# Optimization experiments

Measured on AMD Instinct MI355X. Metric: run time of the kernel, lower is better.

Reference implementation:

```python
import jax, jax.numpy as jnp
import numpy as np

B, S, E, H, K, V = 2, 2048, 2048, 16, 128, 128
EPS = 1e-5


def _rotate(x, cos, sin):
    half = K // 2
    swapped = jnp.concatenate((x[..., half:], x[..., :half]), axis=-1)
    return cos * x + sin * swapped


def setup_inputs() -> dict:
    key = jax.random.key(0)
    k1, k2, k3 = jax.random.split(key, 3)
    embeddings = jax.random.normal(k1, (B, S, E), jnp.float32)
    pos = jnp.arange(S, dtype=jnp.float32)[:, None]
    inv_freq = 1.0 / (10000.0 ** (jnp.arange(0, K, 2, dtype=jnp.float32) / K))
    ang = pos * inv_freq[None, :]
    ang = jnp.concatenate((ang, ang), axis=-1)
    cosb = jnp.cos(ang)[None, None, :, :]
    sinb = jnp.sin(ang)[None, None, :, :]
    cos_buffer = jnp.stack((cosb, cosb))
    sin_buffer = jnp.stack((sinb, sinb))
    causal_buffer = jnp.tril(jnp.ones((S, S), dtype=bool))[None, None]
    w_norm = jnp.ones((E,), jnp.float32)
    w_qkv = jax.random.normal(k2, (E, 2 * K * H + V * H), jnp.float32) * 0.02
    w_out = jax.random.normal(k3, (H * V, E), jnp.float32) * 0.02
    return dict(embeddings=embeddings, cos_buffer=cos_buffer, sin_buffer=sin_buffer,
                causal_buffer=causal_buffer, w_norm=w_norm, w_qkv=w_qkv, w_out=w_out)


def reference(embeddings, cos_buffer, sin_buffer, causal_buffer, w_norm, w_qkv, w_out):
    ms = jnp.mean(embeddings * embeddings, axis=-1, keepdims=True)
    normed = embeddings * jax.lax.rsqrt(ms + EPS) * w_norm
    qkv = normed @ w_qkv
    ks = K * H
    q = qkv[..., :ks].reshape(B, S, H, K).transpose(0, 2, 1, 3)
    k = qkv[..., ks:2 * ks].reshape(B, S, H, K).transpose(0, 2, 1, 3)
    v = qkv[..., 2 * ks:].reshape(B, S, H, V).transpose(0, 2, 1, 3)
    present_k, present_v = k, v
    q = _rotate(q, cos_buffer[0], sin_buffer[0])
    k = _rotate(k, cos_buffer[1], sin_buffer[1])
    scores = jnp.einsum('bhqk,bhsk->bhqs', q, k) / np.float32(np.sqrt(K))
    scores = jnp.where(causal_buffer, scores, -jnp.inf)
    attn = jax.nn.softmax(scores, axis=-1)
    out = jnp.einsum('bhqs,bhsv->bhqv', attn, v)
    out = out.transpose(0, 2, 1, 3).reshape(B, S, H * V) @ w_out
    return embeddings + out, present_k, present_v
```

## Files before the change

kernel.cpp:

```cpp
#include <hip/hip_runtime.h>

typedef unsigned short u16;
typedef unsigned int   u32;
typedef short bf16x8 __attribute__((ext_vector_type(8)));
typedef float f32x4  __attribute__((ext_vector_type(4)));
typedef float f4     __attribute__((ext_vector_type(4)));
typedef u16   u16x4  __attribute__((ext_vector_type(4)));
typedef u16   u16x8  __attribute__((ext_vector_type(8)));

__device__ __forceinline__ u16 f2bf(float x) {
  u32 u = __float_as_uint(x);
  u += 0x7fff + ((u >> 16) & 1);
  return (u16)(u >> 16);
}
__device__ __forceinline__ float bf2f(u16 h) {
  return __uint_as_float(((u32)h) << 16);
}
__device__ __forceinline__ void gload16(const void* g, void* l) {
  __builtin_amdgcn_global_load_lds((const __attribute__((address_space(1))) u32*)g,
                                   (__attribute__((address_space(3))) u32*)l, 16, 0, 0);
}
__device__ __forceinline__ f32x4 mfma16(bf16x8 a, bf16x8 b, f32x4 c) {
  return __builtin_amdgcn_mfma_f32_16x16x32_bf16(a, b, c, 0, 0, 0);
}

__global__ __launch_bounds__(256) void k_rmsnorm(const float* __restrict__ x,
                                                 const float* __restrict__ w,
                                                 u16* __restrict__ out) {
  const int row = blockIdx.x, tid = threadIdx.x;
  const float* xr = x + (size_t)row * 2048;
  f4 a = *(const f4*)&xr[tid * 8];
  f4 b = *(const f4*)&xr[tid * 8 + 4];
  float ss = a[0]*a[0]+a[1]*a[1]+a[2]*a[2]+a[3]*a[3]+b[0]*b[0]+b[1]*b[1]+b[2]*b[2]+b[3]*b[3];
#pragma unroll
  for (int off = 32; off > 0; off >>= 1) ss += __shfl_xor(ss, off);
  __shared__ float red[4];
  if ((tid & 63) == 0) red[tid >> 6] = ss;
  __syncthreads();
  ss = red[0] + red[1] + red[2] + red[3];
  const float sc = rsqrtf(ss * (1.0f / 2048.0f) + 1e-5f);
  f4 wa = *(const f4*)&w[tid * 8];
  f4 wb = *(const f4*)&w[tid * 8 + 4];
  u16x8 o;
#pragma unroll
  for (int i = 0; i < 4; ++i) o[i] = f2bf(a[i] * sc * wa[i]);
#pragma unroll
  for (int i = 0; i < 4; ++i) o[4 + i] = f2bf(b[i] * sc * wb[i]);
  *(u16x8*)&out[(size_t)row * 2048 + tid * 8] = o;
}

__global__ __launch_bounds__(256) void k_transpose_cvt(const float* __restrict__ src,
                                                       u16* __restrict__ dst,
                                                       int R, int C) {
  __shared__ float t[32][33];
  const int tid = threadIdx.x;
  const size_t zoff = (size_t)blockIdx.z * (size_t)R * (size_t)C;
  src += zoff; dst += zoff;
  const int r0 = blockIdx.y * 32, c0 = blockIdx.x * 32;
  const int rr = tid >> 3, cc = (tid & 7) * 4;
  f4 v = *(const f4*)&src[(size_t)(r0 + rr) * C + c0 + cc];
  t[rr][cc] = v[0]; t[rr][cc + 1] = v[1]; t[rr][cc + 2] = v[2]; t[rr][cc + 3] = v[3];
  __syncthreads();
  const int oc = tid >> 3, orr = (tid & 7) * 4;
  u16x4 o;
#pragma unroll
  for (int k = 0; k < 4; ++k) o[k] = f2bf(t[orr + k][oc]);
  *(u16x4*)&dst[(size_t)(c0 + oc) * R + r0 + orr] = o;
}

template <int EPI>
__global__ __launch_bounds__(256) void k_gemm128(
    const u16* __restrict__ A, const u16* __restrict__ Bt,
    u16* __restrict__ q_pre, float* __restrict__ outK, float* __restrict__ outV,
    const float* __restrict__ emb, float* __restrict__ out0,
    u16* __restrict__ vtf) {
  constexpr int KD = 2048;
  __shared__ __align__(16) u16 lA[128 * 64];
  __shared__ __align__(16) u16 lB[128 * 64];
  const int tid = threadIdx.x;
  const int lane = tid & 63;
  const int w = tid >> 6;
  const int wr = w >> 1, wc = w & 1;
  const int g = lane >> 4, c15 = lane & 15;
  const int m0 = blockIdx.y * 128, n0 = blockIdx.x * 128;
  f32x4 acc[4][4] = {};
  for (int kt = 0; kt < KD / 64; ++kt) {
    __syncthreads();
#pragma unroll
    for (int p = 0; p < 4; ++p) {
      int c = p * 256 + tid;
      int row = c >> 3, ch = c & 7;
      int gch = ch ^ (row & 7);
      gload16(&A[(size_t)(m0 + row) * KD + kt * 64 + gch * 8], &lA[c * 8]);
      gload16(&Bt[(size_t)(n0 + row) * KD + kt * 64 + gch * 8], &lB[c * 8]);
    }
    __syncthreads();
#pragma unroll
    for (int ks = 0; ks < 2; ++ks) {
      bf16x8 af[4], bfr[4];
#pragma unroll
      for (int i = 0; i < 4; ++i) {
        int row = wr * 64 + i * 16 + c15;
        int chn = (ks * 4 + g) ^ (row & 7);
        af[i] = *(const bf16x8*)&lA[row * 64 + chn * 8];
      }
#pragma unroll
      for (int j = 0; j < 4; ++j) {
        int row = wc * 64 + j * 16 + c15;
        int chn = (ks * 4 + g) ^ (row & 7);
        bfr[j] = *(const bf16x8*)&lB[row * 64 + chn * 8];
      }
#pragma unroll
      for (int i = 0; i < 4; ++i)
#pragma unroll
        for (int j = 0; j < 4; ++j)
          acc[i][j] = mfma16(af[i], bfr[j], acc[i][j]);
    }
  }
  const int rb = m0 + wr * 64 + g * 4;
  const int cb = wc * 64 + c15;
  if (EPI == 0) {
    const int sec = n0 >> 11;
    const int h = (n0 & 2047) >> 7;
#pragma unroll
    for (int i = 0; i < 4; ++i)
#pragma unroll
      for (int j = 0; j < 4; ++j) {
        const int d = cb + j * 16;
        const int mb = rb + i * 16;
        const int b_ = mb >> 11, s0 = mb & 2047;
#pragma unroll
        for (int r = 0; r < 4; ++r) {
          size_t o = ((size_t)(b_ * 16 + h) * 2048 + (s0 + r)) * 128 + d;
          float val = acc[i][j][r];
          if (sec == 0)      q_pre[o] = f2bf(val);
          else if (sec == 1) outK[o] = val;
          else               outV[o] = val;
        }
        if (sec == 2 && vtf != nullptr) {
          u16x4 vt;
#pragma unroll
          for (int r = 0; r < 4; ++r) vt[r] = f2bf(acc[i][j][r]);
          *(u16x4*)&vtf[((size_t)(b_ * 16 + h) * 128 + d) * 2048 + s0] = vt;
        }
      }
  } else {
#pragma unroll
    for (int i = 0; i < 4; ++i)
#pragma unroll
      for (int j = 0; j < 4; ++j)
#pragma unroll
        for (int r = 0; r < 4; ++r) {
          int mm = rb + i * 16 + r;
          int nn = n0 + cb + j * 16;
          size_t o = (size_t)mm * 2048 + nn;
          out0[o] = acc[i][j][r] + emb[o];
        }
  }
}

__global__ __launch_bounds__(256) void k_rope(const u16* __restrict__ qp,
                                              const float* __restrict__ kp,
                                              const float* __restrict__ cosb,
                                              const float* __restrict__ sinb,
                                              u16* __restrict__ qr, u16* __restrict__ kr) {
  const int gid = blockIdx.x * 256 + threadIdx.x;
  const int row = gid >> 4;
  const int d0 = (gid & 15) * 4;
  const int s = row & 2047;
  const float SC = 0.08838834764831845f;
  const float* c1 = cosb + (size_t)s * 128;
  const float* s1 = sinb + (size_t)s * 128;
  const float* c2 = c1 + 262144;
  const float* s2 = s1 + 262144;
  const size_t base = (size_t)row * 128;
  f4 cl = *(const f4*)&c1[d0], ch = *(const f4*)&c1[d0 + 64];
  f4 sl = *(const f4*)&s1[d0], sh = *(const f4*)&s1[d0 + 64];
  {
    u16x4 xl = *(const u16x4*)&qp[base + d0];
    u16x4 xh = *(const u16x4*)&qp[base + d0 + 64];
    u16x4 ol, oh;
#pragma unroll
    for (int i = 0; i < 4; ++i) {
      float lo = bf2f(xl[i]), hi = bf2f(xh[i]);
      ol[i] = f2bf((cl[i] * lo + sl[i] * hi) * SC);
      oh[i] = f2bf((ch[i] * hi + sh[i] * lo) * SC);
    }
    *(u16x4*)&qr[base + d0] = ol;
    *(u16x4*)&qr[base + d0 + 64] = oh;
  }
  {
    f4 c2l = *(const f4*)&c2[d0], c2h = *(const f4*)&c2[d0 + 64];
    f4 s2l = *(const f4*)&s2[d0], s2h = *(const f4*)&s2[d0 + 64];
    f4 xl = *(const f4*)&kp[base + d0];
    f4 xh = *(const f4*)&kp[base + d0 + 64];
    u16x4 ol, oh;
#pragma unroll
    for (int i = 0; i < 4; ++i) {
      ol[i] = f2bf(c2l[i] * xl[i] + s2l[i] * xh[i]);
      oh[i] = f2bf(c2h[i] * xh[i] + s2h[i] * xl[i]);
    }
    *(u16x4*)&kr[base + d0] = ol;
    *(u16x4*)&kr[base + d0 + 64] = oh;
  }
}

__device__ __forceinline__ void stage_kv(const u16* kb, const u16* vb, int kv0,
                                         u16* dK, u16* dV, int tid) {
#pragma unroll
  for (int p = 0; p < 4; ++p) {
    int c = p * 256 + tid;
    { int row = c >> 4, ch = c & 15, gch = ch ^ (row & 7);
      gload16(&kb[(size_t)(kv0 + row) * 128 + gch * 8], &dK[c * 8]); }
    { int row = c >> 3, ch = c & 7, gch = ch ^ (row & 7);
      gload16(&vb[(size_t)row * 2048 + kv0 + gch * 8], &dV[c * 8]); }
  }
}

__global__ __launch_bounds__(256) void k_attn(const u16* __restrict__ q_rot,
                                              const u16* __restrict__ k_rot,
                                              const u16* __restrict__ v_t,
                                              u16* __restrict__ attn_o) {
  const int bh = blockIdx.y;
  const int b = bh >> 4, h = bh & 15;
  const int tid = threadIdx.x, w = tid >> 6, lane = tid & 63;
  const int g = lane >> 4, c15 = lane & 15;
  __shared__ __align__(16) u16 lK[2][64 * 128];
  __shared__ __align__(16) u16 lV[2][128 * 64];
  __shared__ __align__(16) u16 lP[4][16 * 64];

  const u16* qb = q_rot + (size_t)bh * 2048 * 128;
  const u16* kb = k_rot + (size_t)bh * 2048 * 128;
  const u16* vb = v_t + (size_t)bh * 128 * 2048;
  const float L2E = 1.442695040888963f;
  const float SHIFT = 11.541560327111707f;

  for (int halfp = 0; halfp < 2; ++halfp) {
    const int qt = halfp ? (int)blockIdx.x : 31 - (int)blockIdx.x;
    const int q0 = qt * 64;
    const int nt = qt + 1;

    bf16x8 qf[4];
    const int qrow = q0 + w * 16 + c15;
#pragma unroll
    for (int f = 0; f < 4; ++f)
      qf[f] = *(const bf16x8*)&qb[(size_t)qrow * 128 + f * 32 + g * 8];

    f32x4 O[8];
#pragma unroll
    for (int i = 0; i < 8; ++i) O[i] = {0.f, 0.f, 0.f, 0.f};
    float l[4] = {0.f, 0.f, 0.f, 0.f};
    const int qg = q0 + w * 16 + g * 4;

    stage_kv(kb, vb, 0, &lK[0][0], &lV[0][0], tid);
    asm volatile("s_waitcnt vmcnt(0)" ::: "memory");
    __builtin_amdgcn_s_barrier();

    int cur = 0;
    for (int t = 0; t < nt; ++t) {
      if (t + 1 < nt)
        stage_kv(kb, vb, (t + 1) * 64, &lK[cur ^ 1][0], &lV[cur ^ 1][0], tid);

      const int kv0 = t * 64;
      f32x4 S[4];
#pragma unroll
      for (int n = 0; n < 4; ++n) S[n] = {0.f, 0.f, 0.f, 0.f};
      __builtin_amdgcn_s_setprio(1);
#pragma unroll
      for (int ks = 0; ks < 4; ++ks) {
#pragma unroll
        for (int n = 0; n < 4; ++n) {
          int row = n * 16 + c15;
          int chn = (ks * 4 + g) ^ (row & 7);
          bf16x8 kf = *(const bf16x8*)&lK[cur][row * 128 + chn * 8];
          S[n] = mfma16(qf[ks], kf, S[n]);
        }
      }
      __builtin_amdgcn_s_setprio(0);

      if (t == nt - 1) {
#pragma unroll
        for (int n = 0; n < 4; ++n)
#pragma unroll
          for (int r = 0; r < 4; ++r)
            if (kv0 + n * 16 + c15 > qg + r) S[n][r] = -1e30f;
      }
#pragma unroll
      for (int n = 0; n < 4; ++n)
#pragma unroll
        for (int r = 0; r < 4; ++r) {
          float p = exp2f(__builtin_fmaf(S[n][r], L2E, -SHIFT));
          l[r] += p;
          int qq = g * 4 + r;
          int kv = n * 16 + c15;
          int ch2 = (kv >> 3) ^ (qq & 7);
          lP[w][qq * 64 + ch2 * 8 + (kv & 7)] = f2bf(p);
        }

      __builtin_amdgcn_s_setprio(1);
#pragma unroll
      for (int ks = 0; ks < 2; ++ks) {
        int ch2 = (ks * 4 + g) ^ (c15 & 7);
        bf16x8 pf = *(const bf16x8*)&lP[w][c15 * 64 + ch2 * 8];
#pragma unroll
        for (int nn = 0; nn < 8; ++nn) {
          int row = nn * 16 + c15;
          int chn = (ks * 4 + g) ^ (row & 7);
          bf16x8 vf = *(const bf16x8*)&lV[cur][row * 64 + chn * 8];
          O[nn] = mfma16(pf, vf, O[nn]);
        }
      }
      __builtin_amdgcn_s_setprio(0);

      asm volatile("s_waitcnt vmcnt(0)" ::: "memory");
      __builtin_amdgcn_s_barrier();
      cur ^= 1;
    }

    float inv[4];
#pragma unroll
    for (int r = 0; r < 4; ++r) {
      float t1 = l[r];
#pragma unroll
      for (int off = 1; off < 16; off <<= 1) t1 += __shfl_xor(t1, off);
      inv[r] = 1.0f / t1;
    }
#pragma unroll
    for (int nn = 0; nn < 8; ++nn)
#pragma unroll
      for (int r = 0; r < 4; ++r) {
        int s_ = q0 + w * 16 + g * 4 + r;
        int col = h * 128 + nn * 16 + c15;
        attn_o[(size_t)(b * 2048 + s_) * 2048 + col] = f2bf(O[nn][r] * inv[r]);
      }
  }
}

extern "C" void kernel_launch(void* const* d_in, const int* in_sizes, int n_in,
                              void* d_out, int out_size, void* d_ws, size_t ws_size,
                              hipStream_t stream) {
  const float* emb    = (const float*)d_in[0];
  const float* cosb   = (const float*)d_in[1];
  const float* sinb   = (const float*)d_in[2];
  const float* w_norm = (const float*)d_in[4];
  const float* w_qkv  = (const float*)d_in[5];
  const float* w_out  = (const float*)d_in[6];

  float* out0 = (float*)d_out;
  float* outK = out0 + 8388608;
  float* outV = out0 + 16777216;

  char* ws = (char*)d_ws;
  u16* normed = (u16*)(ws + 0);
  u16* wqkvT  = (u16*)(ws + 16777216);
  u16* woutT  = (u16*)(ws + 41943040);
  u16* q_pre  = (u16*)(ws + 50331648);
  u16* q_rot  = (u16*)(ws + 67108864);
  u16* k_rot  = (u16*)(ws + 83886080);
  u16* attn_o = normed;

  const bool fuse_vt = ws_size >= (size_t)117440512;
  u16* v_t = fuse_vt ? (u16*)(ws + 100663296) : wqkvT;

  k_rmsnorm<<<4096, 256, 0, stream>>>(emb, w_norm, normed);
  k_transpose_cvt<<<dim3(192, 64, 1), 256, 0, stream>>>(w_qkv, wqkvT, 2048, 6144);
  k_transpose_cvt<<<dim3(64, 64, 1), 256, 0, stream>>>(w_out, woutT, 2048, 2048);
  k_gemm128<0><<<dim3(48, 32), 256, 0, stream>>>(normed, wqkvT, q_pre, outK, outV,
                                                 nullptr, nullptr,
                                                 fuse_vt ? v_t : nullptr);
  k_rope<<<4096, 256, 0, stream>>>(q_pre, outK, cosb, sinb, q_rot, k_rot);
  if (!fuse_vt)
    k_transpose_cvt<<<dim3(4, 64, 32), 256, 0, stream>>>(outV, v_t, 2048, 128);
  k_attn<<<dim3(16, 32), 256, 0, stream>>>(q_rot, k_rot, v_t, attn_o);
  k_gemm128<1><<<dim3(16, 32), 256, 0, stream>>>(attn_o, woutT, nullptr, nullptr, nullptr,
                                                 emb, out0, nullptr);
}
```

Baseline: 304.1 us.

## Replace QKV GEMM with 256x256-tile 8-wave double-buffered pipelined kernel

Adds a new GEMM kernel using 512 threads (8 waves) with 256x256 output tiles, double-buffered LDS staging via direct global-to-LDS loads, XOR-swizzled layout, and interleaved prefetch with MFMA quarters guarded by barriers and s_setprio. It replaces the 128x128 GEMM for the QKV projection. The aim is more data reuse per tile and overlap of memory loads with matrix math. In exchange it uses 128KB of LDS per block, and the grid shrinks to 384 blocks, which may leave some compute units underused.

```diff
diff --git a/kernel.cpp b/kernel.cpp
--- a/kernel.cpp
+++ b/kernel.cpp
@@ -66,6 +66,145 @@
 #pragma unroll
   for (int k = 0; k < 4; ++k) o[k] = f2bf(t[orr + k][oc]);
   *(u16x4*)&dst[(size_t)(c0 + oc) * R + r0 + orr] = o;
+}
+
+#define GBAR() __builtin_amdgcn_s_barrier()
+
+#define LOADA(S, Q)                                                             \
+  _Pragma("unroll") for (int di = 0; di < 2; ++di)                              \
+  _Pragma("unroll") for (int kk = 0; kk < 2; ++kk)                              \
+    a2[di][kk] = *(const bf16x8*)&lA[S][wm][((2*(Q)+di)*16 + c15)*64 + (((kk*4+g)^xo)*8)];
+
+#define LOADB(S)                                                                \
+  _Pragma("unroll") for (int j = 0; j < 4; ++j)                                 \
+  _Pragma("unroll") for (int kk = 0; kk < 2; ++kk)                              \
+    b2[j][kk] = *(const bf16x8*)&lB[S][wn>>1][(brow0 + j*16 + c15)*64 + (((kk*4+g)^xo)*8)];
+
+#define MFMAQ(Q)                                                                \
+  __builtin_amdgcn_s_setprio(1);                                                \
+  _Pragma("unroll") for (int di = 0; di < 2; ++di)                              \
+  _Pragma("unroll") for (int j = 0; j < 4; ++j)                                 \
+  _Pragma("unroll") for (int kk = 0; kk < 2; ++kk)                              \
+    acc[2*(Q)+di][j] = mfma16(a2[di][kk], b2[j][kk], acc[2*(Q)+di][j]);         \
+  __builtin_amdgcn_s_setprio(0);
+
+template <int EPI>
+__global__ __launch_bounds__(512, 2) void k_gemm8p(
+    const u16* __restrict__ A, const u16* __restrict__ Bt,
+    u16* __restrict__ q_pre, float* __restrict__ outK, float* __restrict__ outV,
+    const float* __restrict__ emb, float* __restrict__ out0,
+    u16* __restrict__ vtf) {
+  constexpr int NT = 32;
+  __shared__ __align__(16) u16 lA[2][2][128 * 64];
+  __shared__ __align__(16) u16 lB[2][2][128 * 64];
+  const int tid = threadIdx.x;
+  const int lane = tid & 63;
+  const int w = tid >> 6;
+  const int wm = w >> 2, wn = w & 3;
+  const int g = lane >> 4, c15 = lane & 15;
+  const int m0 = blockIdx.y * 256, n0 = blockIdx.x * 256;
+  const int brow0 = (wn & 1) * 64;
+  const int xo = c15 & 7;
+  const int srow = tid >> 3, sch = tid & 7;
+
+  f32x4 acc[8][4] = {};
+  bf16x8 a2[2][2], b2[4][2];
+
+  auto stgA = [&](int t, int hf, int band) {
+    int row = band * 64 + srow;
+    int gch = sch ^ (row & 7);
+    gload16(&A[(size_t)(m0 + hf * 128 + row) * 2048 + t * 64 + gch * 8],
+            &lA[t & 1][hf][row * 64 + sch * 8]);
+  };
+  auto stgB = [&](int t, int hf, int band) {
+    int row = band * 64 + srow;
+    int gch = sch ^ (row & 7);
+    gload16(&Bt[(size_t)(n0 + hf * 128 + row) * 2048 + t * 64 + gch * 8],
+            &lB[t & 1][hf][row * 64 + sch * 8]);
+  };
+
+  stgA(0, 0, 0); stgA(0, 0, 1); stgA(0, 1, 0); stgA(0, 1, 1);
+  stgB(0, 0, 0); stgB(0, 0, 1); stgB(0, 1, 0); stgB(0, 1, 1);
+  stgB(1, 0, 0); stgB(1, 0, 1); stgB(1, 1, 0); stgB(1, 1, 1);
+  stgA(1, 0, 0); stgA(1, 1, 0);
+  asm volatile("s_waitcnt vmcnt(6)" ::: "memory");
+  GBAR();
+
+  for (int tp = 0; tp < NT; tp += 2) {
+    const bool pf2 = (tp + 2 < NT);
+    const bool pf3 = (tp + 3 < NT);
+    LOADB(0); LOADA(0, 0);
+    stgA(tp + 1, 0, 1); stgA(tp + 1, 1, 1);
+    GBAR(); MFMAQ(0); GBAR();
+    LOADA(0, 1);
+    if (pf2) { stgB(tp + 2, 0, 0); stgB(tp + 2, 0, 1); }
+    GBAR(); MFMAQ(1); GBAR();
+    LOADA(0, 2);
+    if (pf2) { stgB(tp + 2, 1, 0); stgB(tp + 2, 1, 1); }
+    GBAR(); MFMAQ(2); GBAR();
+    LOADA(0, 3);
+    if (pf2) { stgA(tp + 2, 0, 0); stgA(tp + 2, 1, 0); }
+    GBAR(); MFMAQ(3);
+    if (pf2) asm volatile("s_waitcnt vmcnt(6)" ::: "memory");
+    else     asm volatile("s_waitcnt vmcnt(0)" ::: "memory");
+    GBAR();
+    LOADB(1); LOADA(1, 0);
+    if (pf2) { stgA(tp + 2, 0, 1); stgA(tp + 2, 1, 1); }
+    GBAR(); MFMAQ(0); GBAR();
+    LOADA(1, 1);
+    if (pf3) { stgB(tp + 3, 0, 0); stgB(tp + 3, 0, 1); }
+    GBAR(); MFMAQ(1); GBAR();
+    LOADA(1, 2);
+    if (pf3) { stgB(tp + 3, 1, 0); stgB(tp + 3, 1, 1); }
+    GBAR(); MFMAQ(2); GBAR();
+    LOADA(1, 3);
+    if (pf3) { stgA(tp + 3, 0, 0); stgA(tp + 3, 1, 0); }
+    GBAR(); MFMAQ(3);
+    if (pf2) asm volatile("s_waitcnt vmcnt(6)" ::: "memory");
+    else     asm volatile("s_waitcnt vmcnt(0)" ::: "memory");
+    GBAR();
+  }
+
+  const int rbase = m0 + wm * 128;
+  const int cbase = wn * 64;
+  if (EPI == 0) {
+    const int sec = n0 >> 11;
+#pragma unroll
+    for (int i = 0; i < 8; ++i)
+#pragma unroll
+      for (int j = 0; j < 4; ++j) {
+        int colq = (n0 & 2047) + cbase + j * 16 + c15;
+        int h = colq >> 7, d = colq & 127;
+        int mm0 = rbase + i * 16 + g * 4;
+        int b_ = mm0 >> 11, s0 = mm0 & 2047;
+#pragma unroll
+        for (int r = 0; r < 4; ++r) {
+          size_t o = ((size_t)(b_ * 16 + h) * 2048 + (s0 + r)) * 128 + d;
+          float val = acc[i][j][r];
+          if (sec == 0)      q_pre[o] = f2bf(val);
+          else if (sec == 1) outK[o] = val;
+          else               outV[o] = val;
+        }
+        if (sec == 2 && vtf != nullptr) {
+          u16x4 vt;
+#pragma unroll
+          for (int r = 0; r < 4; ++r) vt[r] = f2bf(acc[i][j][r]);
+          *(u16x4*)&vtf[((size_t)(b_ * 16 + h) * 128 + d) * 2048 + s0] = vt;
+        }
+      }
+  } else {
+#pragma unroll
+    for (int i = 0; i < 8; ++i)
+#pragma unroll
+      for (int j = 0; j < 4; ++j)
+#pragma unroll
+        for (int r = 0; r < 4; ++r) {
+          int mm = rbase + i * 16 + g * 4 + r;
+          int nn = n0 + cbase + j * 16 + c15;
+          size_t o = (size_t)mm * 2048 + nn;
+          out0[o] = acc[i][j][r] + emb[o];
+        }
+  }
 }
 
 template <int EPI>
@@ -365,9 +504,9 @@
   k_rmsnorm<<<4096, 256, 0, stream>>>(emb, w_norm, normed);
   k_transpose_cvt<<<dim3(192, 64, 1), 256, 0, stream>>>(w_qkv, wqkvT, 2048, 6144);
   k_transpose_cvt<<<dim3(64, 64, 1), 256, 0, stream>>>(w_out, woutT, 2048, 2048);
-  k_gemm128<0><<<dim3(48, 32), 256, 0, stream>>>(normed, wqkvT, q_pre, outK, outV,
-                                                 nullptr, nullptr,
-                                                 fuse_vt ? v_t : nullptr);
+  k_gemm8p<0><<<dim3(24, 16), 512, 0, stream>>>(normed, wqkvT, q_pre, outK, outV,
+                                                nullptr, nullptr,
+                                                fuse_vt ? v_t : nullptr);
   k_rope<<<4096, 256, 0, stream>>>(q_pre, outK, cosb, sinb, q_rot, k_rot);
   if (!fuse_vt)
     k_transpose_cvt<<<dim3(4, 64, 32), 256, 0, stream>>>(outV, v_t, 2048, 128);
```

After: 311.7 us. 1.02x slower.
